# Kernel tuning notes

Hardware: AMD Instinct MI355X
Metric: run time of the kernel (lower is better)

Reference implementation:

```python
import jax, jax.numpy as jnp
import numpy as np

B = 16
N_IN_PER = 256
N_SKIP_PER = 1024
C_IN = 256
C_SKIP = 128


def setup_inputs() -> dict:
    key = jax.random.key(0)
    ks = jax.random.split(key, 8)
    n_in = B * N_IN_PER
    n_skip = B * N_SKIP_PER
    in_x = jax.random.normal(ks[0], (n_in, C_IN), dtype=jnp.float32)
    in_pos = jax.random.uniform(ks[1], (n_in, 3), dtype=jnp.float32)
    in_batch = jnp.repeat(jnp.arange(B, dtype=jnp.int64), N_IN_PER)
    skip_x = jax.random.normal(ks[2], (n_skip, C_SKIP), dtype=jnp.float32)
    skip_pos = jax.random.uniform(ks[3], (n_skip, 3), dtype=jnp.float32)
    skip_batch = jnp.repeat(jnp.arange(B, dtype=jnp.int64), N_SKIP_PER)
    d_cat = C_IN + C_SKIP + 3  # 387
    W1 = jax.random.normal(ks[4], (d_cat, 256), dtype=jnp.float32) * (1.0 / np.sqrt(d_cat))
    b1 = jnp.zeros((256,), dtype=jnp.float32)
    W2 = jax.random.normal(ks[5], (256, 256), dtype=jnp.float32) * (1.0 / 16.0)
    b2 = jnp.zeros((256,), dtype=jnp.float32)
    return {"in_x": in_x, "in_pos": in_pos, "in_batch": in_batch,
            "skip_x": skip_x, "skip_pos": skip_pos, "skip_batch": skip_batch,
            "W1": W1, "b1": b1, "W2": W2, "b2": b2, "knn_num": 3}


def _knn_interpolate(in_x, in_pos, in_batch, skip_pos, skip_batch, k):
    # Pairwise squared distances fine->coarse, masked across graphs. [Ns, Ni]
    d2 = jnp.sum((skip_pos[:, None, :] - in_pos[None, :, :]) ** 2, axis=-1)
    cross = skip_batch[:, None] != in_batch[None, :]
    d2 = jnp.where(cross, jnp.inf, d2)
    _, idx = jax.lax.top_k(-d2, k)  # [Ns, k] nearest coarse neighbors
    nb_pos = in_pos[idx]  # [Ns, k, 3]
    dist = jnp.sqrt(jnp.sum((nb_pos - skip_pos[:, None, :]) ** 2, axis=-1))
    dist = jnp.maximum(dist, 1e-10)
    w = 1.0 / dist
    w = w / (jnp.sum(w, axis=-1, keepdims=True) + 1e-16)  # per-target normalization
    return jnp.einsum('nk,nkc->nc', w, in_x[idx])  # [Ns, C_in]


def reference(in_x, in_pos, in_batch, skip_x, skip_pos, skip_batch, W1, b1, W2, b2, knn_num):
    interp = _knn_interpolate(in_x, in_pos, in_batch, skip_pos, skip_batch, knn_num)
    h = jnp.concatenate([interp, skip_x, skip_pos], axis=1)  # [Ns, 387]
    h = jax.nn.relu(h @ W1 + b1)
    h = jax.nn.relu(h @ W2 + b2)
    return h
```

## Files before the change

### kernel.cpp

```cpp
#include <hip/hip_runtime.h>
#include <hip/hip_bf16.h>


typedef __bf16 bf16x8 __attribute__((ext_vector_type(8)));
typedef float  f32x4  __attribute__((ext_vector_type(4)));

__device__ __forceinline__ unsigned short f2bf(float f) {
  __hip_bfloat16 h = __float2bfloat16(f);
  return __builtin_bit_cast(unsigned short, h);
}

#define GLDS16(G, L)                                                          \
  __builtin_amdgcn_global_load_lds(                                           \
      (const __attribute__((address_space(1))) void*)(G),                     \
      (__attribute__((address_space(3))) void*)(L), 16, 0, 0)

#define BAR()    __builtin_amdgcn_s_barrier()
#define WAITV(N) asm volatile("s_waitcnt vmcnt(" #N ")" ::: "memory")
#define WAITL()  asm volatile("s_waitcnt lgkmcnt(0)" ::: "memory")

static constexpr int MROWS = 16384;
static constexpr int KPAD  = 416;
static constexpr int KREAL = 387;

__global__ __launch_bounds__(256) void prep_w(
    const float* __restrict__ W1, const float* __restrict__ W2,
    unsigned short* __restrict__ W1t, unsigned short* __restrict__ W2t)
{
  __shared__ float T[64][65];
  int b = blockIdx.x;
  const float* S; unsigned short* D; int KP, Kreal, kb, nb;
  if (b < 28) { S = W1; D = W1t; KP = KPAD; Kreal = KREAL; kb = b >> 2; nb = b & 3; }
  else { b -= 28; S = W2; D = W2t; KP = 256; Kreal = 256; kb = b >> 2; nb = b & 3; }
  const int k0 = kb << 6, n0 = nb << 6;
  const int tr = threadIdx.x >> 4, tc = threadIdx.x & 15;
#pragma unroll
  for (int i = 0; i < 4; ++i) {
    const int k = k0 + i * 16 + tr;
    float4 v = make_float4(0.f, 0.f, 0.f, 0.f);
    if (k < Kreal) v = *(const float4*)(S + (size_t)k * 256 + n0 + tc * 4);
    T[i * 16 + tr][tc * 4 + 0] = v.x;
    T[i * 16 + tr][tc * 4 + 1] = v.y;
    T[i * 16 + tr][tc * 4 + 2] = v.z;
    T[i * 16 + tr][tc * 4 + 3] = v.w;
  }
  __syncthreads();
#pragma unroll
  for (int i = 0; i < 4; ++i) {
    const int n = n0 + i * 16 + tr;
    const int k = k0 + tc * 4;
    if (k < KP) {
      ushort4 o;
      o.x = f2bf(T[tc * 4 + 0][i * 16 + tr]);
      o.y = f2bf(T[tc * 4 + 1][i * 16 + tr]);
      o.z = f2bf(T[tc * 4 + 2][i * 16 + tr]);
      o.w = f2bf(T[tc * 4 + 3][i * 16 + tr]);
      *(ushort4*)(D + (size_t)n * KP + k) = o;
    }
  }
}

__global__ __launch_bounds__(256) void knn_h(
    const float* __restrict__ in_x,
    const float* __restrict__ in_pos,
    const float* __restrict__ skip_x,
    const float* __restrict__ skip_pos,
    unsigned short* __restrict__ H)
{
  __shared__ float P[3][256];
  const int tid = threadIdx.x;
  const int s0  = blockIdx.x << 2;
  const int ib  = (s0 >> 10) << 8;
  {
    const float* bp = in_pos + (size_t)ib * 3;
    for (int i = tid; i < 768; i += 256) P[i % 3][i / 3] = bp[i];
  }
  __syncthreads();

  const int wid = tid >> 6, lane = tid & 63;
  const int s = s0 + wid;
  const float sx = skip_pos[(size_t)s * 3 + 0];
  const float sy = skip_pos[(size_t)s * 3 + 1];
  const float sz = skip_pos[(size_t)s * 3 + 2];

  float d2[4];
#pragma unroll
  for (int q = 0; q < 4; ++q) {
    const int i = lane + (q << 6);
    const float dx = __fsub_rn(sx, P[0][i]);
    const float dy = __fsub_rn(sy, P[1][i]);
    const float dz = __fsub_rn(sz, P[2][i]);
    d2[q] = __fadd_rn(__fadd_rn(__fmul_rn(dx, dx), __fmul_rn(dy, dy)),
                      __fmul_rn(dz, dz));
  }

  int   gsel[3];
  float wsel[3];
  float wsum = 0.f;
#pragma unroll
  for (int p = 0; p < 3; ++p) {
    float bd = d2[0];
    int   bi = lane;
#pragma unroll
    for (int q = 1; q < 4; ++q) {
      const int i = lane + (q << 6);
      if (d2[q] < bd) { bd = d2[q]; bi = i; }
    }
#pragma unroll
    for (int m = 1; m < 64; m <<= 1) {
      const float od = __shfl_xor(bd, m);
      const int   oi = __shfl_xor(bi, m);
      if (od < bd || (od == bd && oi < bi)) { bd = od; bi = oi; }
    }
    const bool win = ((bi & 63) == lane);
    const int  qw  = bi >> 6;
    d2[0] = (win && qw == 0) ? 3.4e38f : d2[0];
    d2[1] = (win && qw == 1) ? 3.4e38f : d2[1];
    d2[2] = (win && qw == 2) ? 3.4e38f : d2[2];
    d2[3] = (win && qw == 3) ? 3.4e38f : d2[3];
    gsel[p] = bi;
    const float w = 1.0f / fmaxf(sqrtf(bd), 1e-10f);
    wsel[p] = w;
    wsum += w;
  }
  const float denom = wsum + 1e-16f;
  const float w0 = wsel[0] / denom;
  const float w1 = wsel[1] / denom;
  const float w2 = wsel[2] / denom;

  const f32x4 a = *(const f32x4*)(in_x + (size_t)(ib + gsel[0]) * 256 + lane * 4);
  const f32x4 b = *(const f32x4*)(in_x + (size_t)(ib + gsel[1]) * 256 + lane * 4);
  const f32x4 c = *(const f32x4*)(in_x + (size_t)(ib + gsel[2]) * 256 + lane * 4);

  unsigned short* hr = H + (size_t)s * KPAD;
  ushort4 o4;
  o4.x = f2bf(w0 * a.x + w1 * b.x + w2 * c.x);
  o4.y = f2bf(w0 * a.y + w1 * b.y + w2 * c.y);
  o4.z = f2bf(w0 * a.z + w1 * b.z + w2 * c.z);
  o4.w = f2bf(w0 * a.w + w1 * b.w + w2 * c.w);
  *(ushort4*)(hr + (lane << 2)) = o4;

  const float2 sv = ((const float2*)(skip_x + (size_t)s * 128))[lane];
  ushort2 o2;
  o2.x = f2bf(sv.x);
  o2.y = f2bf(sv.y);
  *(ushort2*)(hr + 256 + (lane << 1)) = o2;

  if (lane < 32) {
    float v = (lane == 0) ? sx : (lane == 1) ? sy : (lane == 2) ? sz : 0.f;
    hr[384 + lane] = f2bf(v);
  }
}

template <int K, int NK, bool OUT_BF16>
__global__ __launch_bounds__(256) void gemm_p3(
    const unsigned short* __restrict__ A,
    const unsigned short* __restrict__ Bt,
    const float* __restrict__ bias,
    void* __restrict__ Out)
{
  __shared__ unsigned short As[4][128 * 32];
  __shared__ unsigned short Bs[4][128 * 32];
  const int tid = threadIdx.x, lane = tid & 63, wid = tid >> 6;
  const int m0 = blockIdx.x << 7, n0 = blockIdx.y << 7;
  const int fr = lane & 15, g = lane >> 4;
  const int wr = (wid >> 1) << 6, wcc = (wid & 1) << 6;

  const int r  = tid >> 2;
  const int cs = (tid & 3) ^ ((r >> 1) & 3);
  const unsigned short* gA0 = A + (size_t)(m0 + r) * K + cs * 8;
  const unsigned short* gA1 = gA0 + (size_t)64 * K;
  const unsigned short* gB0 = Bt + (size_t)(n0 + r) * K + cs * 8;
  const unsigned short* gB1 = gB0 + (size_t)64 * K;

#define STAGE(ks, b)                                                          \
  {                                                                           \
    const int _ko = (ks) * 32;                                                \
    GLDS16(gA0 + _ko, &As[b][wid * 512]);                                     \
    GLDS16(gA1 + _ko, &As[b][2048 + wid * 512]);                              \
    GLDS16(gB0 + _ko, &Bs[b][wid * 512]);                                     \
    GLDS16(gB1 + _ko, &Bs[b][2048 + wid * 512]);                              \
  }

  int woff[4], hoff[4];
#pragma unroll
  for (int i = 0; i < 4; ++i) {
    const int Rw = wcc + i * 16 + fr;
    const int Rh = wr + i * 16 + fr;
    woff[i] = Rw * 32 + ((g ^ ((Rw >> 1) & 3)) << 3);
    hoff[i] = Rh * 32 + ((g ^ ((Rh >> 1) & 3)) << 3);
  }

  STAGE(0, 0); STAGE(1, 1); STAGE(2, 2);

  f32x4 acc[4][4] = {};

#pragma unroll 1
  for (int ks = 0; ks < NK; ++ks) {
    if (ks + 3 < NK) STAGE(ks + 3, (ks + 3) & 3);
    const int rem = NK - 1 - ks;
    if (rem >= 3)      { WAITV(12); }
    else if (rem == 2) { WAITV(8); }
    else if (rem == 1) { WAITV(4); }
    else               { WAITV(0); }
    BAR();
    const unsigned short* as = As[ks & 3];
    const unsigned short* bs = Bs[ks & 3];
    bf16x8 wf[4], hf[4];
#pragma unroll
    for (int i = 0; i < 4; ++i) wf[i] = *(const bf16x8*)&bs[woff[i]];
#pragma unroll
    for (int i = 0; i < 4; ++i) hf[i] = *(const bf16x8*)&as[hoff[i]];
#pragma unroll
    for (int mc = 0; mc < 4; ++mc)
#pragma unroll
      for (int rr = 0; rr < 4; ++rr)
        acc[mc][rr] = __builtin_amdgcn_mfma_f32_16x16x32_bf16(
            wf[mc], hf[rr], acc[mc][rr], 0, 0, 0);
    WAITL(); BAR();
  }
#undef STAGE

  f32x4 bv[4];
#pragma unroll
  for (int mc = 0; mc < 4; ++mc)
    bv[mc] = *(const f32x4*)(bias + n0 + wcc + mc * 16 + g * 4);
#pragma unroll
  for (int rr = 0; rr < 4; ++rr) {
    const size_t row = (size_t)(m0 + wr + rr * 16 + fr);
#pragma unroll
    for (int mc = 0; mc < 4; ++mc) {
      const int col = n0 + wcc + mc * 16 + g * 4;
      if constexpr (OUT_BF16) {
        ushort4 o;
        o.x = f2bf(fmaxf(acc[mc][rr][0] + bv[mc][0], 0.f));
        o.y = f2bf(fmaxf(acc[mc][rr][1] + bv[mc][1], 0.f));
        o.z = f2bf(fmaxf(acc[mc][rr][2] + bv[mc][2], 0.f));
        o.w = f2bf(fmaxf(acc[mc][rr][3] + bv[mc][3], 0.f));
        *(ushort4*)((unsigned short*)Out + row * 256 + col) = o;
      } else {
        f32x4 o;
#pragma unroll
        for (int j = 0; j < 4; ++j) o[j] = fmaxf(acc[mc][rr][j] + bv[mc][j], 0.f);
        *(f32x4*)((float*)Out + row * 256 + col) = o;
      }
    }
  }
}

extern "C" void kernel_launch(void* const* d_in, const int* in_sizes, int n_in,
                              void* d_out, int out_size, void* d_ws, size_t ws_size,
                              hipStream_t stream) {
  const float* in_x     = (const float*)d_in[0];
  const float* in_pos   = (const float*)d_in[1];
  const float* skip_x   = (const float*)d_in[3];
  const float* skip_pos = (const float*)d_in[4];
  const float* W1       = (const float*)d_in[6];
  const float* bias1    = (const float*)d_in[7];
  const float* W2       = (const float*)d_in[8];
  const float* bias2    = (const float*)d_in[9];

  char* ws = (char*)d_ws;
  unsigned short* W1t = (unsigned short*)(ws);
  unsigned short* W2t = (unsigned short*)(ws + 212992);
  unsigned short* H   = (unsigned short*)(ws + 212992 + 131072);
  unsigned short* h1  = (unsigned short*)(ws + 212992 + 131072 + 13631488);

  prep_w<<<dim3(44), dim3(256), 0, stream>>>(W1, W2, W1t, W2t);
  knn_h<<<dim3(MROWS / 4), dim3(256), 0, stream>>>(in_x, in_pos, skip_x,
                                                   skip_pos, H);
  gemm_p3<KPAD, 13, true><<<dim3(MROWS / 128, 2), dim3(256), 0, stream>>>(
      H, W1t, bias1, (void*)h1);
  gemm_p3<256, 8, false><<<dim3(MROWS / 128, 2), dim3(256), 0, stream>>>(
      h1, W2t, bias2, d_out);
}
```

Baseline: 47.48 us.

## Fuse both MLP GEMMs into one kernel with h1 kept in LDS

Merges the weight-prep kernel into the kNN kernel as extra blocks, and fuses the two GEMMs into a single kernel. Each block computes 64 rows across all 256 output columns, keeps the bf16 hidden activation h1 in shared memory, then runs the second GEMM from LDS. This removes two launches and the global write and read of h1. In exchange the M tile shrinks to 64, which means more weight traffic per row, larger LDS use (roughly 113KB) and fewer blocks (256), so occupancy may drop.

```diff
diff --git a/kernel.cpp b/kernel.cpp
--- a/kernel.cpp
+++ b/kernel.cpp
@@ -22,55 +22,59 @@
 static constexpr int MROWS = 16384;
 static constexpr int KPAD  = 416;
 static constexpr int KREAL = 387;
-
-__global__ __launch_bounds__(256) void prep_w(
-    const float* __restrict__ W1, const float* __restrict__ W2,
-    unsigned short* __restrict__ W1t, unsigned short* __restrict__ W2t)
-{
-  __shared__ float T[64][65];
-  int b = blockIdx.x;
-  const float* S; unsigned short* D; int KP, Kreal, kb, nb;
-  if (b < 28) { S = W1; D = W1t; KP = KPAD; Kreal = KREAL; kb = b >> 2; nb = b & 3; }
-  else { b -= 28; S = W2; D = W2t; KP = 256; Kreal = 256; kb = b >> 2; nb = b & 3; }
-  const int k0 = kb << 6, n0 = nb << 6;
-  const int tr = threadIdx.x >> 4, tc = threadIdx.x & 15;
-#pragma unroll
-  for (int i = 0; i < 4; ++i) {
-    const int k = k0 + i * 16 + tr;
-    float4 v = make_float4(0.f, 0.f, 0.f, 0.f);
-    if (k < Kreal) v = *(const float4*)(S + (size_t)k * 256 + n0 + tc * 4);
-    T[i * 16 + tr][tc * 4 + 0] = v.x;
-    T[i * 16 + tr][tc * 4 + 1] = v.y;
-    T[i * 16 + tr][tc * 4 + 2] = v.z;
-    T[i * 16 + tr][tc * 4 + 3] = v.w;
-  }
-  __syncthreads();
-#pragma unroll
-  for (int i = 0; i < 4; ++i) {
-    const int n = n0 + i * 16 + tr;
-    const int k = k0 + tc * 4;
-    if (k < KP) {
-      ushort4 o;
-      o.x = f2bf(T[tc * 4 + 0][i * 16 + tr]);
-      o.y = f2bf(T[tc * 4 + 1][i * 16 + tr]);
-      o.z = f2bf(T[tc * 4 + 2][i * 16 + tr]);
-      o.w = f2bf(T[tc * 4 + 3][i * 16 + tr]);
-      *(ushort4*)(D + (size_t)n * KP + k) = o;
-    }
-  }
-}
-
-__global__ __launch_bounds__(256) void knn_h(
+static constexpr int NK1   = 13;
+static constexpr int NK2   = 8;
+static constexpr int H1STR = 264;
+
+__global__ __launch_bounds__(256) void knn_prep(
     const float* __restrict__ in_x,
     const float* __restrict__ in_pos,
     const float* __restrict__ skip_x,
     const float* __restrict__ skip_pos,
+    const float* __restrict__ W1, const float* __restrict__ W2,
+    unsigned short* __restrict__ W1t, unsigned short* __restrict__ W2t,
     unsigned short* __restrict__ H)
 {
+  __shared__ float T[64][65];
   __shared__ float P[3][256];
   const int tid = threadIdx.x;
-  const int s0  = blockIdx.x << 2;
-  const int ib  = (s0 >> 10) << 8;
+
+  if (blockIdx.x < 44) {
+    int b = blockIdx.x;
+    const float* S; unsigned short* D; int KP, Kreal, kb, nb;
+    if (b < 28) { S = W1; D = W1t; KP = KPAD; Kreal = KREAL; kb = b >> 2; nb = b & 3; }
+    else { b -= 28; S = W2; D = W2t; KP = 256; Kreal = 256; kb = b >> 2; nb = b & 3; }
+    const int k0 = kb << 6, n0 = nb << 6;
+    const int tr = tid >> 4, tc = tid & 15;
+#pragma unroll
+    for (int i = 0; i < 4; ++i) {
+      const int k = k0 + i * 16 + tr;
+      float4 v = make_float4(0.f, 0.f, 0.f, 0.f);
+      if (k < Kreal) v = *(const float4*)(S + (size_t)k * 256 + n0 + tc * 4);
+      T[i * 16 + tr][tc * 4 + 0] = v.x;
+      T[i * 16 + tr][tc * 4 + 1] = v.y;
+      T[i * 16 + tr][tc * 4 + 2] = v.z;
+      T[i * 16 + tr][tc * 4 + 3] = v.w;
+    }
+    __syncthreads();
+#pragma unroll
+    for (int i = 0; i < 4; ++i) {
+      const int n = n0 + i * 16 + tr;
+      const int k = k0 + tc * 4;
+      if (k < KP) {
+        ushort4 o;
+        o.x = f2bf(T[tc * 4 + 0][i * 16 + tr]);
+        o.y = f2bf(T[tc * 4 + 1][i * 16 + tr]);
+        o.z = f2bf(T[tc * 4 + 2][i * 16 + tr]);
+        o.w = f2bf(T[tc * 4 + 3][i * 16 + tr]);
+        *(ushort4*)(D + (size_t)n * KP + k) = o;
+      }
+    }
+    return;
+  }
+
+  const int s0 = (blockIdx.x - 44) << 2;
+  const int ib = (s0 >> 10) << 8;
   {
     const float* bp = in_pos + (size_t)ib * 3;
     for (int i = tid; i < 768; i += 256) P[i % 3][i / 3] = bp[i];
@@ -94,13 +98,10 @@
                       __fmul_rn(dz, dz));
   }
 
-  int   gsel[3];
-  float wsel[3];
-  float wsum = 0.f;
+  int gsel[3]; float wsel[3]; float wsum = 0.f;
 #pragma unroll
   for (int p = 0; p < 3; ++p) {
-    float bd = d2[0];
-    int   bi = lane;
+    float bd = d2[0]; int bi = lane;
 #pragma unroll
     for (int q = 1; q < 4; ++q) {
       const int i = lane + (q << 6);
@@ -120,8 +121,7 @@
     d2[3] = (win && qw == 3) ? 3.4e38f : d2[3];
     gsel[p] = bi;
     const float w = 1.0f / fmaxf(sqrtf(bd), 1e-10f);
-    wsel[p] = w;
-    wsum += w;
+    wsel[p] = w; wsum += w;
   }
   const float denom = wsum + 1e-16f;
   const float w0 = wsel[0] / denom;
@@ -141,9 +141,7 @@
   *(ushort4*)(hr + (lane << 2)) = o4;
 
   const float2 sv = ((const float2*)(skip_x + (size_t)s * 128))[lane];
-  ushort2 o2;
-  o2.x = f2bf(sv.x);
-  o2.y = f2bf(sv.y);
+  ushort2 o2; o2.x = f2bf(sv.x); o2.y = f2bf(sv.y);
   *(ushort2*)(hr + 256 + (lane << 1)) = o2;
 
   if (lane < 32) {
@@ -152,65 +150,127 @@
   }
 }
 
-template <int K, int NK, bool OUT_BF16>
-__global__ __launch_bounds__(256) void gemm_p3(
-    const unsigned short* __restrict__ A,
-    const unsigned short* __restrict__ Bt,
-    const float* __restrict__ bias,
-    void* __restrict__ Out)
+__global__ __launch_bounds__(256) void gemm12(
+    const unsigned short* __restrict__ Hg,
+    const unsigned short* __restrict__ W1t,
+    const unsigned short* __restrict__ W2t,
+    const float* __restrict__ bias1, const float* __restrict__ bias2,
+    float* __restrict__ out)
 {
-  __shared__ unsigned short As[4][128 * 32];
-  __shared__ unsigned short Bs[4][128 * 32];
+  __shared__ unsigned short As[4][64 * 32];
+  __shared__ unsigned short Bs[4][256 * 32];
+  __shared__ unsigned short h1s[64 * H1STR];
+
   const int tid = threadIdx.x, lane = tid & 63, wid = tid >> 6;
-  const int m0 = blockIdx.x << 7, n0 = blockIdx.y << 7;
+  const int m0 = blockIdx.x << 6;
   const int fr = lane & 15, g = lane >> 4;
-  const int wr = (wid >> 1) << 6, wcc = (wid & 1) << 6;
+  const int wcc = wid << 6;
 
   const int r  = tid >> 2;
   const int cs = (tid & 3) ^ ((r >> 1) & 3);
-  const unsigned short* gA0 = A + (size_t)(m0 + r) * K + cs * 8;
-  const unsigned short* gA1 = gA0 + (size_t)64 * K;
-  const unsigned short* gB0 = Bt + (size_t)(n0 + r) * K + cs * 8;
-  const unsigned short* gB1 = gB0 + (size_t)64 * K;
-
-#define STAGE(ks, b)                                                          \
+  const unsigned short* gA   = Hg  + (size_t)(m0 + r) * KPAD + cs * 8;
+  const unsigned short* gB10 = W1t + (size_t)r * KPAD + cs * 8;
+  const unsigned short* gB20 = W2t + (size_t)r * 256  + cs * 8;
+
+#define STAGE1(ks, bu)                                                        \
   {                                                                           \
     const int _ko = (ks) * 32;                                                \
-    GLDS16(gA0 + _ko, &As[b][wid * 512]);                                     \
-    GLDS16(gA1 + _ko, &As[b][2048 + wid * 512]);                              \
-    GLDS16(gB0 + _ko, &Bs[b][wid * 512]);                                     \
-    GLDS16(gB1 + _ko, &Bs[b][2048 + wid * 512]);                              \
-  }
-
-  int woff[4], hoff[4];
+    GLDS16(gA + _ko, &As[bu][wid * 512]);                                     \
+    GLDS16(gB10 + _ko,                 &Bs[bu][wid * 512]);                   \
+    GLDS16(gB10 + 64 * KPAD + _ko,     &Bs[bu][2048 + wid * 512]);            \
+    GLDS16(gB10 + 128 * KPAD + _ko,    &Bs[bu][4096 + wid * 512]);            \
+    GLDS16(gB10 + 192 * KPAD + _ko,    &Bs[bu][6144 + wid * 512]);            \
+  }
+#define STAGE2(ks, bu)                                                        \
+  {                                                                           \
+    const int _ko = (ks) * 32;                                                \
+    GLDS16(gB20 + _ko,                 &Bs[bu][wid * 512]);                   \
+    GLDS16(gB20 + 64 * 256 + _ko,      &Bs[bu][2048 + wid * 512]);            \
+    GLDS16(gB20 + 128 * 256 + _ko,     &Bs[bu][4096 + wid * 512]);            \
+    GLDS16(gB20 + 192 * 256 + _ko,     &Bs[bu][6144 + wid * 512]);            \
+  }
+
+  STAGE1(0, 0); STAGE1(1, 1); STAGE1(2, 2);
+
+  int woff[4], hoff[4], h2off[4];
 #pragma unroll
   for (int i = 0; i < 4; ++i) {
     const int Rw = wcc + i * 16 + fr;
-    const int Rh = wr + i * 16 + fr;
-    woff[i] = Rw * 32 + ((g ^ ((Rw >> 1) & 3)) << 3);
-    hoff[i] = Rh * 32 + ((g ^ ((Rh >> 1) & 3)) << 3);
-  }
-
-  STAGE(0, 0); STAGE(1, 1); STAGE(2, 2);
+    const int Rh = i * 16 + fr;
+    woff[i]  = Rw * 32 + ((g ^ ((Rw >> 1) & 3)) << 3);
+    hoff[i]  = Rh * 32 + ((g ^ ((Rh >> 1) & 3)) << 3);
+    h2off[i] = Rh * H1STR + g * 8;
+  }
+
+  f32x4 bv1[4], bv2[4];
+#pragma unroll
+  for (int mc = 0; mc < 4; ++mc) {
+    bv1[mc] = *(const f32x4*)(bias1 + wcc + mc * 16 + g * 4);
+    bv2[mc] = *(const f32x4*)(bias2 + wcc + mc * 16 + g * 4);
+  }
 
   f32x4 acc[4][4] = {};
 
 #pragma unroll 1
-  for (int ks = 0; ks < NK; ++ks) {
-    if (ks + 3 < NK) STAGE(ks + 3, (ks + 3) & 3);
-    const int rem = NK - 1 - ks;
+  for (int ks = 0; ks < NK1; ++ks) {
+    if (ks + 3 < NK1) STAGE1(ks + 3, (ks + 3) & 3);
+    const int rem = NK1 - 1 - ks;
+    if (rem >= 3)      { WAITV(15); }
+    else if (rem == 2) { WAITV(10); }
+    else if (rem == 1) { WAITV(5); }
+    else               { WAITV(0); }
+    BAR();
+    const unsigned short* as = As[ks & 3];
+    const unsigned short* bs = Bs[ks & 3];
+    bf16x8 wf[4], hf[4];
+#pragma unroll
+    for (int i = 0; i < 4; ++i) wf[i] = *(const bf16x8*)&bs[woff[i]];
+#pragma unroll
+    for (int i = 0; i < 4; ++i) hf[i] = *(const bf16x8*)&as[hoff[i]];
+#pragma unroll
+    for (int mc = 0; mc < 4; ++mc)
+#pragma unroll
+      for (int rr = 0; rr < 4; ++rr)
+        acc[mc][rr] = __builtin_amdgcn_mfma_f32_16x16x32_bf16(
+            wf[mc], hf[rr], acc[mc][rr], 0, 0, 0);
+    WAITL(); BAR();
+  }
+
+  STAGE2(0, 0); STAGE2(1, 1); STAGE2(2, 2);
+
+#pragma unroll
+  for (int rr = 0; rr < 4; ++rr)
+#pragma unroll
+    for (int mc = 0; mc < 4; ++mc) {
+      ushort4 o;
+      o.x = f2bf(fmaxf(acc[mc][rr][0] + bv1[mc][0], 0.f));
+      o.y = f2bf(fmaxf(acc[mc][rr][1] + bv1[mc][1], 0.f));
+      o.z = f2bf(fmaxf(acc[mc][rr][2] + bv1[mc][2], 0.f));
+      o.w = f2bf(fmaxf(acc[mc][rr][3] + bv1[mc][3], 0.f));
+      *(ushort4*)&h1s[(rr * 16 + fr) * H1STR + wcc + mc * 16 + g * 4] = o;
+    }
+  WAITL(); BAR();
+
+#pragma unroll
+  for (int mc = 0; mc < 4; ++mc)
+#pragma unroll
+    for (int rr = 0; rr < 4; ++rr) acc[mc][rr] = f32x4{0.f, 0.f, 0.f, 0.f};
+
+#pragma unroll 1
+  for (int ks = 0; ks < NK2; ++ks) {
+    if (ks + 3 < NK2) STAGE2(ks + 3, (ks + 3) & 3);
+    const int rem = NK2 - 1 - ks;
     if (rem >= 3)      { WAITV(12); }
     else if (rem == 2) { WAITV(8); }
     else if (rem == 1) { WAITV(4); }
     else               { WAITV(0); }
     BAR();
-    const unsigned short* as = As[ks & 3];
     const unsigned short* bs = Bs[ks & 3];
     bf16x8 wf[4], hf[4];
 #pragma unroll
     for (int i = 0; i < 4; ++i) wf[i] = *(const bf16x8*)&bs[woff[i]];
 #pragma unroll
-    for (int i = 0; i < 4; ++i) hf[i] = *(const bf16x8*)&as[hoff[i]];
+    for (int i = 0; i < 4; ++i) hf[i] = *(const bf16x8*)&h1s[h2off[i] + ks * 32];
 #pragma unroll
     for (int mc = 0; mc < 4; ++mc)
 #pragma unroll
@@ -219,31 +279,18 @@
             wf[mc], hf[rr], acc[mc][rr], 0, 0, 0);
     WAITL(); BAR();
   }
-#undef STAGE
-
-  f32x4 bv[4];
-#pragma unroll
-  for (int mc = 0; mc < 4; ++mc)
-    bv[mc] = *(const f32x4*)(bias + n0 + wcc + mc * 16 + g * 4);
+#undef STAGE1
+#undef STAGE2
+
 #pragma unroll
   for (int rr = 0; rr < 4; ++rr) {
-    const size_t row = (size_t)(m0 + wr + rr * 16 + fr);
+    const size_t row = (size_t)(m0 + rr * 16 + fr);
 #pragma unroll
     for (int mc = 0; mc < 4; ++mc) {
-      const int col = n0 + wcc + mc * 16 + g * 4;
-      if constexpr (OUT_BF16) {
-        ushort4 o;
-        o.x = f2bf(fmaxf(acc[mc][rr][0] + bv[mc][0], 0.f));
-        o.y = f2bf(fmaxf(acc[mc][rr][1] + bv[mc][1], 0.f));
-        o.z = f2bf(fmaxf(acc[mc][rr][2] + bv[mc][2], 0.f));
-        o.w = f2bf(fmaxf(acc[mc][rr][3] + bv[mc][3], 0.f));
-        *(ushort4*)((unsigned short*)Out + row * 256 + col) = o;
-      } else {
-        f32x4 o;
-#pragma unroll
-        for (int j = 0; j < 4; ++j) o[j] = fmaxf(acc[mc][rr][j] + bv[mc][j], 0.f);
-        *(f32x4*)((float*)Out + row * 256 + col) = o;
-      }
+      f32x4 o;
+#pragma unroll
+      for (int j = 0; j < 4; ++j) o[j] = fmaxf(acc[mc][rr][j] + bv2[mc][j], 0.f);
+      *(f32x4*)(out + row * 256 + wcc + mc * 16 + g * 4) = o;
     }
   }
 }
@@ -264,13 +311,9 @@
   unsigned short* W1t = (unsigned short*)(ws);
   unsigned short* W2t = (unsigned short*)(ws + 212992);
   unsigned short* H   = (unsigned short*)(ws + 212992 + 131072);
-  unsigned short* h1  = (unsigned short*)(ws + 212992 + 131072 + 13631488);
-
-  prep_w<<<dim3(44), dim3(256), 0, stream>>>(W1, W2, W1t, W2t);
-  knn_h<<<dim3(MROWS / 4), dim3(256), 0, stream>>>(in_x, in_pos, skip_x,
-                                                   skip_pos, H);
-  gemm_p3<KPAD, 13, true><<<dim3(MROWS / 128, 2), dim3(256), 0, stream>>>(
-      H, W1t, bias1, (void*)h1);
-  gemm_p3<256, 8, false><<<dim3(MROWS / 128, 2), dim3(256), 0, stream>>>(
-      h1, W2t, bias2, d_out);
+
+  knn_prep<<<dim3(44 + MROWS / 4), dim3(256), 0, stream>>>(
+      in_x, in_pos, skip_x, skip_pos, W1, W2, W1t, W2t, H);
+  gemm12<<<dim3(MROWS / 64), dim3(256), 0, stream>>>(
+      H, W1t, W2t, bias1, bias2, (float*)d_out);
 }
```

After: 40.28 us. -15.2%, faster.
